# Kernel tuning notes

Measured on AMD Instinct MI355X. Metric: run time of the kernel, lower is better.

## Reference

```python
import jax, jax.numpy as jnp
import numpy as np
from jax import lax

INPUT, HIDDEN, OUT = 5, 32, 2

def setup_inputs() -> dict:
    key = jax.random.key(0)
    ks = jax.random.split(key, 7)
    s_ih = 1.0 / np.sqrt(HIDDEN)
    return {
        "x": jax.random.normal(ks[0], (16384, 200, INPUT), dtype=jnp.float32),
        "W_ih": jax.random.uniform(ks[1], (4 * HIDDEN, INPUT), jnp.float32, -s_ih, s_ih),
        "W_hh": jax.random.uniform(ks[2], (4 * HIDDEN, HIDDEN), jnp.float32, -s_ih, s_ih),
        "b_ih": jax.random.uniform(ks[3], (4 * HIDDEN,), jnp.float32, -s_ih, s_ih),
        "b_hh": jax.random.uniform(ks[4], (4 * HIDDEN,), jnp.float32, -s_ih, s_ih),
        "W_fc": jax.random.uniform(ks[5], (OUT, HIDDEN), jnp.float32, -s_ih, s_ih),
        "b_fc": jax.random.uniform(ks[6], (OUT,), jnp.float32, -s_ih, s_ih),
    }

def reference(x, W_ih, W_hh, b_ih, b_hh, W_fc, b_fc):
    B = x.shape[0]
    # Precompute input projections for all timesteps in one GEMM: [B,T,4H]
    x_proj = jnp.einsum("bti,gi->btg", x, W_ih) + (b_ih + b_hh)
    xs = jnp.swapaxes(x_proj, 0, 1)  # [T, B, 4H]

    def step(carry, xg):
        h, c = carry
        gates = xg + h @ W_hh.T  # [B, 4H]
        i, f, g, o = jnp.split(gates, 4, axis=-1)  # torch gate order i,f,g,o
        i = jax.nn.sigmoid(i)
        f = jax.nn.sigmoid(f)
        g = jnp.tanh(g)
        o = jax.nn.sigmoid(o)
        c = f * c + i * g
        h = o * jnp.tanh(c)
        return (h, c), None

    h0 = jnp.zeros((B, HIDDEN), x.dtype)
    c0 = jnp.zeros((B, HIDDEN), x.dtype)
    (h_n, _), _ = lax.scan(step, (h0, c0), xs)
    return h_n @ W_fc.T + b_fc  # [B, 2]
```

## Files before the change

kernel.cpp:

```cpp
#include <hip/hip_runtime.h>


typedef __bf16 bf16x8 __attribute__((ext_vector_type(8)));
typedef float  f32x4  __attribute__((ext_vector_type(4)));
typedef float  f32x2  __attribute__((ext_vector_type(2)));
typedef unsigned int u32;

constexpr int kT = 200, kIN = 5, kH = 32;
constexpr int CT = 40;

constexpr float kL  = 1.4426950408889634f;
constexpr float k2L = 2.8853900817779268f;

union FragU { bf16x8 v; __bf16 b[8]; unsigned short s[8]; u32 u[4]; uint4 q4; };

__device__ __forceinline__ unsigned short bfbits(__bf16 b) {
    union { __bf16 b; unsigned short s; } u; u.b = b; return u.s;
}
__device__ __forceinline__ void split2(float x, __bf16& hi, __bf16& lo) {
    hi = (__bf16)x;
    lo = (__bf16)(x - (float)hi);
}
__device__ __forceinline__ u32 pkbf(float a, float b) {
    return (u32)bfbits((__bf16)a) | ((u32)bfbits((__bf16)b) << 16);
}
__device__ __forceinline__ float f_from_bits(u32 x) {
    union { u32 u; float f; } t; t.u = x; return t.f;
}

__global__ __launch_bounds__(64) void lstm_reg9(
    const float* __restrict__ x,
    const float* __restrict__ W_ih,
    const float* __restrict__ W_hh,
    const float* __restrict__ b_ih,
    const float* __restrict__ b_hh,
    const float* __restrict__ W_fc,
    const float* __restrict__ b_fc,
    float* __restrict__ out)
{
    __shared__ uint4 xbuf[CT][34];

    const int lane = threadIdx.x;
    const int n16  = lane & 15;
    const int q    = lane >> 4;
    const int b0   = blockIdx.x * 16;

    bf16x8 whhA_h[8], whhA_l[8], wihA[8];
#pragma unroll
    for (int t8 = 0; t8 < 8; ++t8) {
        const int g  = t8 & 3, hb = t8 >> 2;
        const int R  = g * 32 + 8 * (n16 >> 2) + 4 * hb + (n16 & 3);
        const float sc = (g == 2) ? k2L : kL;
        FragU H, L;
#pragma unroll
        for (int j = 0; j < 8; ++j)
            split2(sc * W_hh[R * kH + q * 8 + j], H.b[j], L.b[j]);
        whhA_h[t8] = H.v; whhA_l[t8] = L.v;

        float wr[5];
#pragma unroll
        for (int i = 0; i < 5; ++i) wr[i] = sc * W_ih[R * kIN + i];
        __bf16 bh, bl;
        split2(sc * (b_ih[R] + b_hh[R]), bh, bl);

        FragU F;
        F.u[0] = F.u[1] = F.u[2] = F.u[3] = 0u;
        if (q == 0) {
#pragma unroll
            for (int i = 0; i < 5; ++i) F.b[i] = (__bf16)wr[i];
#pragma unroll
            for (int i = 0; i < 3; ++i) F.b[5 + i] = (__bf16)wr[i];
        } else if (q == 1) {
            F.b[0] = (__bf16)wr[3];
            F.b[1] = (__bf16)wr[4];
#pragma unroll
            for (int i = 0; i < 5; ++i) {
                __bf16 hbb, lbb; split2(wr[i], hbb, lbb);
                F.b[2 + i] = lbb;
            }
            F.b[7] = bh;
        } else if (q == 2) {
            F.b[0] = bl;
        }
        wihA[t8] = F.v;
    }

    for (int t2 = lane; t2 < CT; t2 += 64) {
        xbuf[t2][32] = make_uint4(0x3F80u, 0u, 0u, 0u);
        xbuf[t2][33] = make_uint4(0u, 0u, 0u, 0u);
    }

    const int col = (q < 2) ? (n16 * 2 + q) : (30 + q);
    const f32x4 zf4 = {0.f, 0.f, 0.f, 0.f};

    f32x2 c8v[4] = {{0.f, 0.f}, {0.f, 0.f}, {0.f, 0.f}, {0.f, 0.f}};
    FragU Bh, Bl;
    Bh.u[0] = Bh.u[1] = Bh.u[2] = Bh.u[3] = 0u;
    Bl.u[0] = Bl.u[1] = Bl.u[2] = Bl.u[3] = 0u;

    for (int phase = 0; phase < kT / CT; ++phase) {
        {
            const int mm = lane >> 2, pp = lane & 3;
            const float2* xr2 = (const float2*)(x + (size_t)(b0 + mm) * (kT * kIN)
                                                  + (size_t)(phase * CT + pp * 10) * kIN);
            float xv[50];
#pragma unroll
            for (int i = 0; i < 25; ++i) {
                float2 v = xr2[i];
                xv[2 * i] = v.x; xv[2 * i + 1] = v.y;
            }
#pragma unroll
            for (int s5 = 0; s5 < 10; ++s5) {
                u32 xh[5], xl[5];
#pragma unroll
                for (int i = 0; i < 5; ++i) {
                    __bf16 hbb, lbb; split2(xv[s5 * 5 + i], hbb, lbb);
                    xh[i] = bfbits(hbb); xl[i] = bfbits(lbb);
                }
                uint4 f0 = make_uint4(xh[0] | (xh[1] << 16),
                                      xh[2] | (xh[3] << 16),
                                      xh[4] | (xl[0] << 16),
                                      xl[1] | (xl[2] << 16));
                uint4 f1 = make_uint4(xl[3] | (xl[4] << 16),
                                      xh[0] | (xh[1] << 16),
                                      xh[2] | (xh[3] << 16),
                                      xh[4] | (0x3F80u << 16));
                const int tc = pp * 10 + s5;
                xbuf[tc][mm * 2 + 0] = f0;
                xbuf[tc][mm * 2 + 1] = f1;
            }
        }
        __syncthreads();

        FragU xg; xg.q4 = xbuf[0][col];

#pragma unroll 1
        for (int tc = 0; tc < CT; ++tc) {
            FragU xgn;
            const int tn = (tc + 1 < CT) ? tc + 1 : 0;
            xgn.q4 = xbuf[tn][col];

            f32x4 acc[8];
#pragma unroll
            for (int t8 = 0; t8 < 8; ++t8)
                acc[t8] = __builtin_amdgcn_mfma_f32_16x16x32_bf16(wihA[t8], xg.v, zf4, 0, 0, 0);
#pragma unroll
            for (int t8 = 0; t8 < 8; ++t8)
                acc[t8] = __builtin_amdgcn_mfma_f32_16x16x32_bf16(whhA_h[t8], Bh.v, acc[t8], 0, 0, 0);
#pragma unroll
            for (int t8 = 0; t8 < 8; ++t8)
                acc[t8] = __builtin_amdgcn_mfma_f32_16x16x32_bf16(whhA_h[t8], Bl.v, acc[t8], 0, 0, 0);
#pragma unroll
            for (int t8 = 0; t8 < 8; ++t8)
                acc[t8] = __builtin_amdgcn_mfma_f32_16x16x32_bf16(whhA_l[t8], Bh.v, acc[t8], 0, 0, 0);

#pragma unroll
            for (int m2 = 0; m2 < 4; ++m2) {
                const int ti = (m2 >> 1) * 4;
                const int r0 = (m2 & 1) * 2, r1 = r0 + 1;

                f32x2 eu = { __builtin_amdgcn_exp2f(-acc[ti + 0][r0]),
                             __builtin_amdgcn_exp2f(-acc[ti + 0][r1]) };
                f32x2 ew = { __builtin_amdgcn_exp2f(-acc[ti + 1][r0]),
                             __builtin_amdgcn_exp2f(-acc[ti + 1][r1]) };
                f32x2 ev = { __builtin_amdgcn_exp2f(-acc[ti + 2][r0]),
                             __builtin_amdgcn_exp2f(-acc[ti + 2][r1]) };
                f32x2 ep = { __builtin_amdgcn_exp2f(-acc[ti + 3][r0]),
                             __builtin_amdgcn_exp2f(-acc[ti + 3][r1]) };

                f32x2 A = (eu + 1.0f) * (ev + 1.0f);
                f32x2 B = ew + 1.0f;
                float rA = __builtin_amdgcn_rcpf(A.x * A.y);
                float rB = __builtin_amdgcn_rcpf(B.x * B.y);

                f32x2 t;
                t.x = fmaf(ev.x, -k2L, k2L);
                t.y = fmaf(ev.y, -k2L, k2L);

                f32x2 fA = f32x2{A.y, A.x} * rA;
                f32x2 fB = f32x2{B.y, B.x} * rB;
                f32x2 tfA = t * fA;
                f32x2 c;
                c.x = fmaf(c8v[m2].x, fB.x, tfA.x);
                c.y = fmaf(c8v[m2].y, fB.y, tfA.y);
                c.x = fmaxf(c.x, -35.0f);
                c.y = fmaxf(c.y, -35.0f);
                c8v[m2] = c;

                f32x2 es = { __builtin_amdgcn_exp2f(-c.x),
                             __builtin_amdgcn_exp2f(-c.y) };
                f32x2 C = (ep + 1.0f) * (es + 1.0f);
                float rC = __builtin_amdgcn_rcpf(C.x * C.y);
                f32x2 h = (1.0f - es) * (f32x2{C.y, C.x} * rC);

                u32 wh = pkbf(h.x, h.y);
                f32x2 hif = { f_from_bits(wh << 16), f_from_bits(wh & 0xffff0000u) };
                f32x2 lo = h - hif;
                Bh.u[m2] = wh;
                Bl.u[m2] = pkbf(lo.x, lo.y);
            }

            xg = xgn;
        }
    }

    __syncthreads();
    float* hfin = (float*)xbuf;
#pragma unroll
    for (int jj = 0; jj < 8; ++jj)
        hfin[n16 * 33 + q * 8 + jj] = (float)Bh.b[jj] + (float)Bl.b[jj];
    __syncthreads();
    if (lane < 32) {
        const int m = lane >> 1, o = lane & 1;
        float s = b_fc[o];
#pragma unroll
        for (int j = 0; j < kH; ++j)
            s = fmaf(hfin[m * 33 + j], W_fc[o * kH + j], s);
        out[(size_t)(b0 + m) * 2 + o] = s;
    }
}

extern "C" void kernel_launch(void* const* d_in, const int* in_sizes, int n_in,
                              void* d_out, int out_size, void* d_ws, size_t ws_size,
                              hipStream_t stream) {
    const float* x    = (const float*)d_in[0];
    const float* W_ih = (const float*)d_in[1];
    const float* W_hh = (const float*)d_in[2];
    const float* b_ih = (const float*)d_in[3];
    const float* b_hh = (const float*)d_in[4];
    const float* W_fc = (const float*)d_in[5];
    const float* b_fc = (const float*)d_in[6];
    float* out = (float*)d_out;

    hipLaunchKernelGGL(lstm_reg9, dim3(1024), dim3(64), 0, stream,
                       x, W_ih, W_hh, b_ih, b_hh, W_fc, b_fc, out);
}
```

Baseline: 239.5 us.

## Split each LSTM batch tile across two wavefronts exchanging hidden state via LDS

Each 16-sequence block now runs two wavefronts. Each wave owns half of the hidden units and computes its gate MFMAs and activations, cutting per-wave MFMA and transcendental work in half. Each step the waves swap their packed hidden-state halves through a double-buffered LDS exchange and a block barrier. The cost is a __syncthreads and LDS traffic on every timestep of the serial recurrence, and only one wave loads x.

New measurement: 263.3 us. 1.1x slower.

```diff
diff --git a/kernel.cpp b/kernel.cpp
--- a/kernel.cpp
+++ b/kernel.cpp
@@ -28,7 +28,7 @@
     union { u32 u; float f; } t; t.u = x; return t.f;
 }
 
-__global__ __launch_bounds__(64) void lstm_reg9(
+__global__ __launch_bounds__(128) void lstm_dw(
     const float* __restrict__ x,
     const float* __restrict__ W_ih,
     const float* __restrict__ W_hh,
@@ -39,23 +39,25 @@
     float* __restrict__ out)
 {
     __shared__ uint4 xbuf[CT][34];
-
-    const int lane = threadIdx.x;
+    __shared__ uint4 xch[2][2][64];
+
+    const int tid  = threadIdx.x;
+    const int wid  = tid >> 6;
+    const int lane = tid & 63;
     const int n16  = lane & 15;
     const int q    = lane >> 4;
     const int b0   = blockIdx.x * 16;
 
-    bf16x8 whhA_h[8], whhA_l[8], wihA[8];
-#pragma unroll
-    for (int t8 = 0; t8 < 8; ++t8) {
-        const int g  = t8 & 3, hb = t8 >> 2;
-        const int R  = g * 32 + 8 * (n16 >> 2) + 4 * hb + (n16 & 3);
+    bf16x8 whhA_h[4], whhA_l[4], wihA[4];
+#pragma unroll
+    for (int g = 0; g < 4; ++g) {
+        const int R = g * 32 + 8 * (n16 >> 2) + 4 * wid + (n16 & 3);
         const float sc = (g == 2) ? k2L : kL;
         FragU H, L;
 #pragma unroll
         for (int j = 0; j < 8; ++j)
             split2(sc * W_hh[R * kH + q * 8 + j], H.b[j], L.b[j]);
-        whhA_h[t8] = H.v; whhA_l[t8] = L.v;
+        whhA_h[g] = H.v; whhA_l[g] = L.v;
 
         float wr[5];
 #pragma unroll
@@ -82,24 +84,25 @@
         } else if (q == 2) {
             F.b[0] = bl;
         }
-        wihA[t8] = F.v;
-    }
-
-    for (int t2 = lane; t2 < CT; t2 += 64) {
+        wihA[g] = F.v;
+    }
+
+    for (int t2 = tid; t2 < CT; t2 += 128) {
         xbuf[t2][32] = make_uint4(0x3F80u, 0u, 0u, 0u);
         xbuf[t2][33] = make_uint4(0u, 0u, 0u, 0u);
     }
+    xch[0][wid][lane] = make_uint4(0u, 0u, 0u, 0u);
+    xch[1][wid][lane] = make_uint4(0u, 0u, 0u, 0u);
 
     const int col = (q < 2) ? (n16 * 2 + q) : (30 + q);
     const f32x4 zf4 = {0.f, 0.f, 0.f, 0.f};
 
-    f32x2 c8v[4] = {{0.f, 0.f}, {0.f, 0.f}, {0.f, 0.f}, {0.f, 0.f}};
-    FragU Bh, Bl;
-    Bh.u[0] = Bh.u[1] = Bh.u[2] = Bh.u[3] = 0u;
-    Bl.u[0] = Bl.u[1] = Bl.u[2] = Bl.u[3] = 0u;
+    f32x2 c4v[2] = {{0.f, 0.f}, {0.f, 0.f}};
+    u32 bh_own[2] = {0u, 0u};
+    u32 bl_own[2] = {0u, 0u};
 
     for (int phase = 0; phase < kT / CT; ++phase) {
-        {
+        if (wid == 0) {
             const int mm = lane >> 2, pp = lane & 3;
             const float2* xr2 = (const float2*)(x + (size_t)(b0 + mm) * (kT * kIN)
                                                   + (size_t)(phase * CT + pp * 10) * kIN);
@@ -140,33 +143,46 @@
             const int tn = (tc + 1 < CT) ? tc + 1 : 0;
             xgn.q4 = xbuf[tn][col];
 
-            f32x4 acc[8];
-#pragma unroll
-            for (int t8 = 0; t8 < 8; ++t8)
-                acc[t8] = __builtin_amdgcn_mfma_f32_16x16x32_bf16(wihA[t8], xg.v, zf4, 0, 0, 0);
-#pragma unroll
-            for (int t8 = 0; t8 < 8; ++t8)
-                acc[t8] = __builtin_amdgcn_mfma_f32_16x16x32_bf16(whhA_h[t8], Bh.v, acc[t8], 0, 0, 0);
-#pragma unroll
-            for (int t8 = 0; t8 < 8; ++t8)
-                acc[t8] = __builtin_amdgcn_mfma_f32_16x16x32_bf16(whhA_h[t8], Bl.v, acc[t8], 0, 0, 0);
-#pragma unroll
-            for (int t8 = 0; t8 < 8; ++t8)
-                acc[t8] = __builtin_amdgcn_mfma_f32_16x16x32_bf16(whhA_l[t8], Bh.v, acc[t8], 0, 0, 0);
-
-#pragma unroll
-            for (int m2 = 0; m2 < 4; ++m2) {
-                const int ti = (m2 >> 1) * 4;
-                const int r0 = (m2 & 1) * 2, r1 = r0 + 1;
-
-                f32x2 eu = { __builtin_amdgcn_exp2f(-acc[ti + 0][r0]),
-                             __builtin_amdgcn_exp2f(-acc[ti + 0][r1]) };
-                f32x2 ew = { __builtin_amdgcn_exp2f(-acc[ti + 1][r0]),
-                             __builtin_amdgcn_exp2f(-acc[ti + 1][r1]) };
-                f32x2 ev = { __builtin_amdgcn_exp2f(-acc[ti + 2][r0]),
-                             __builtin_amdgcn_exp2f(-acc[ti + 2][r1]) };
-                f32x2 ep = { __builtin_amdgcn_exp2f(-acc[ti + 3][r0]),
-                             __builtin_amdgcn_exp2f(-acc[ti + 3][r1]) };
+            const uint4 oth = xch[(tc ^ 1) & 1][wid ^ 1][lane];
+            FragU BhF, BlF;
+            if (wid == 0) {
+                BhF.u[0] = bh_own[0]; BhF.u[1] = bh_own[1];
+                BhF.u[2] = oth.x;     BhF.u[3] = oth.y;
+                BlF.u[0] = bl_own[0]; BlF.u[1] = bl_own[1];
+                BlF.u[2] = oth.z;     BlF.u[3] = oth.w;
+            } else {
+                BhF.u[0] = oth.x;     BhF.u[1] = oth.y;
+                BhF.u[2] = bh_own[0]; BhF.u[3] = bh_own[1];
+                BlF.u[0] = oth.z;     BlF.u[1] = oth.w;
+                BlF.u[2] = bl_own[0]; BlF.u[3] = bl_own[1];
+            }
+
+            f32x4 acc[4];
+#pragma unroll
+            for (int g = 0; g < 4; ++g)
+                acc[g] = __builtin_amdgcn_mfma_f32_16x16x32_bf16(wihA[g], xg.v, zf4, 0, 0, 0);
+#pragma unroll
+            for (int g = 0; g < 4; ++g)
+                acc[g] = __builtin_amdgcn_mfma_f32_16x16x32_bf16(whhA_h[g], BhF.v, acc[g], 0, 0, 0);
+#pragma unroll
+            for (int g = 0; g < 4; ++g)
+                acc[g] = __builtin_amdgcn_mfma_f32_16x16x32_bf16(whhA_h[g], BlF.v, acc[g], 0, 0, 0);
+#pragma unroll
+            for (int g = 0; g < 4; ++g)
+                acc[g] = __builtin_amdgcn_mfma_f32_16x16x32_bf16(whhA_l[g], BhF.v, acc[g], 0, 0, 0);
+
+#pragma unroll
+            for (int p = 0; p < 2; ++p) {
+                const int r0 = 2 * p, r1 = r0 + 1;
+
+                f32x2 eu = { __builtin_amdgcn_exp2f(-acc[0][r0]),
+                             __builtin_amdgcn_exp2f(-acc[0][r1]) };
+                f32x2 ew = { __builtin_amdgcn_exp2f(-acc[1][r0]),
+                             __builtin_amdgcn_exp2f(-acc[1][r1]) };
+                f32x2 ev = { __builtin_amdgcn_exp2f(-acc[2][r0]),
+                             __builtin_amdgcn_exp2f(-acc[2][r1]) };
+                f32x2 ep = { __builtin_amdgcn_exp2f(-acc[3][r0]),
+                             __builtin_amdgcn_exp2f(-acc[3][r1]) };
 
                 f32x2 A = (eu + 1.0f) * (ev + 1.0f);
                 f32x2 B = ew + 1.0f;
@@ -181,11 +197,11 @@
                 f32x2 fB = f32x2{B.y, B.x} * rB;
                 f32x2 tfA = t * fA;
                 f32x2 c;
-                c.x = fmaf(c8v[m2].x, fB.x, tfA.x);
-                c.y = fmaf(c8v[m2].y, fB.y, tfA.y);
+                c.x = fmaf(c4v[p].x, fB.x, tfA.x);
+                c.y = fmaf(c4v[p].y, fB.y, tfA.y);
                 c.x = fmaxf(c.x, -35.0f);
                 c.y = fmaxf(c.y, -35.0f);
-                c8v[m2] = c;
+                c4v[p] = c;
 
                 f32x2 es = { __builtin_amdgcn_exp2f(-c.x),
                              __builtin_amdgcn_exp2f(-c.y) };
@@ -196,9 +212,13 @@
                 u32 wh = pkbf(h.x, h.y);
                 f32x2 hif = { f_from_bits(wh << 16), f_from_bits(wh & 0xffff0000u) };
                 f32x2 lo = h - hif;
-                Bh.u[m2] = wh;
-                Bl.u[m2] = pkbf(lo.x, lo.y);
-            }
+                bh_own[p] = wh;
+                bl_own[p] = pkbf(lo.x, lo.y);
+            }
+
+            xch[tc & 1][wid][lane] = make_uint4(bh_own[0], bh_own[1],
+                                                bl_own[0], bl_own[1]);
+            __syncthreads();
 
             xg = xgn;
         }
@@ -206,12 +226,17 @@
 
     __syncthreads();
     float* hfin = (float*)xbuf;
-#pragma unroll
-    for (int jj = 0; jj < 8; ++jj)
-        hfin[n16 * 33 + q * 8 + jj] = (float)Bh.b[jj] + (float)Bl.b[jj];
+    {
+        FragU HB, LB;
+        HB.u[0] = bh_own[0]; HB.u[1] = bh_own[1];
+        LB.u[0] = bl_own[0]; LB.u[1] = bl_own[1];
+#pragma unroll
+        for (int jj = 0; jj < 4; ++jj)
+            hfin[n16 * 33 + q * 8 + 4 * wid + jj] = (float)HB.b[jj] + (float)LB.b[jj];
+    }
     __syncthreads();
-    if (lane < 32) {
-        const int m = lane >> 1, o = lane & 1;
+    if (tid < 32) {
+        const int m = tid >> 1, o = tid & 1;
         float s = b_fc[o];
 #pragma unroll
         for (int j = 0; j < kH; ++j)
@@ -232,6 +257,6 @@
     const float* b_fc = (const float*)d_in[6];
     float* out = (float*)d_out;
 
-    hipLaunchKernelGGL(lstm_reg9, dim3(1024), dim3(64), 0, stream,
+    hipLaunchKernelGGL(lstm_dw, dim3(1024), dim3(128), 0, stream,
                        x, W_ih, W_hh, b_ih, b_hh, W_fc, b_fc, out);
 }
```
